# Performance work log

Hardware: AMD Instinct MI355X
Metric: run time of the kernel (lower is better)

## Reference

```python
import jax, jax.numpy as jnp
import numpy as np

N_HEAD, D_K, D_V = 8, 64, 64
TEMP = 20.0
EPS = 1e-12  # F.normalize default eps


def setup_inputs() -> dict:
    key = jax.random.key(0)
    ks = jax.random.split(key, 5)
    bs_q, bs_k, len_q, len_k, d_model = 32, 32, 100, 100, 512
    return {
        "q": jax.random.normal(ks[0], (bs_q, len_q, d_model), jnp.float32),
        "k": jax.random.normal(ks[1], (bs_k, len_k, d_model), jnp.float32),
        "v": jax.random.normal(ks[2], (bs_k, len_k, N_HEAD * D_V), jnp.float32),
        "w_qs": jax.random.normal(ks[3], (N_HEAD * D_K, d_model), jnp.float32) * 0.02,
        "w_ks": jax.random.normal(ks[4], (N_HEAD * D_K, d_model), jnp.float32) * 0.02,
    }


def _l2norm(x):
    return x / jnp.maximum(jnp.linalg.norm(x, axis=-1, keepdims=True), EPS)


def reference(q, k, v, w_qs, w_ks):
    bs_q, len_q, _ = q.shape
    bs_k, len_k, _ = k.shape
    # Linear projections (no bias), then the module's raw view (reshape, no transpose)
    qh = (q @ w_qs.T).reshape(bs_q, N_HEAD, len_q, D_K)
    kh = (k @ w_ks.T).reshape(bs_k, N_HEAD, len_k, D_K)
    vh = v.reshape(bs_k, N_HEAD, len_k, D_V)
    # cosine-similarity scores: L2-normalize q and k along d_k
    qn = _l2norm(qh)
    kn = _l2norm(kh)
    # every q batch element vs every k batch element: [bs_q, bs_k, h, len_q, len_k]
    attn = jnp.einsum("qhld,khmd->qkhlm", qn, kn)
    attn = jax.nn.relu(attn) * TEMP
    attn = jax.nn.softmax(attn, axis=-1)
    out = jnp.einsum("qkhlm,khmd->qkhld", attn, vh)
    # per-i: [bs_k, h, len_q, d_v] -> transpose(1,2) -> reshape, stacked at dim=1
    out = out.transpose(1, 0, 3, 2, 4).reshape(bs_k, bs_q, len_q, N_HEAD * D_V)
    return out
```

## Files before the change

kernel.cpp:

```cpp
#include <hip/hip_runtime.h>
#include <math.h>

typedef short bf16x8 __attribute__((ext_vector_type(8)));
typedef float f32x4  __attribute__((ext_vector_type(4)));
typedef float f32x16 __attribute__((ext_vector_type(16)));
typedef unsigned u32x4 __attribute__((ext_vector_type(4)));

#define TEMP 20.0f

__device__ __forceinline__ ushort f2bf(float f) {
    unsigned u = __float_as_uint(f);
    u = (u + 0x7FFFu + ((u >> 16) & 1u)) >> 16;
    return (ushort)u;
}

__device__ __forceinline__ bf16x8 cvt8(const float4* p) {
    float4 a = p[0], b = p[1];
    bf16x8 r;
    r[0] = (short)f2bf(a.x); r[1] = (short)f2bf(a.y);
    r[2] = (short)f2bf(a.z); r[3] = (short)f2bf(a.w);
    r[4] = (short)f2bf(b.x); r[5] = (short)f2bf(b.y);
    r[6] = (short)f2bf(b.z); r[7] = (short)f2bf(b.w);
    return r;
}

__global__ __launch_bounds__(256) void prep(const float* __restrict__ wq,
                                            const float* __restrict__ wk,
                                            const float* __restrict__ v,
                                            ushort* __restrict__ Wq,
                                            ushort* __restrict__ Wk,
                                            ushort* __restrict__ Vt) {
    __shared__ float T[100 * 65];
    const int b = blockIdx.x, t = threadIdx.x;
    if (b < 256) {
        const float* src = (b < 128) ? wq : wk;
        ushort* dst = (b < 128) ? Wq : Wk;
        const int idx = (b & 127) * 2048 + t * 8;
        *(bf16x8*)(dst + idx) = cvt8((const float4*)(src + idx));
        return;
    }
    const int bb = b - 256;
    const float* in = v + (size_t)(bb >> 3) * 51200 + (bb & 7) * 6400;
    for (int i = t; i < 6400; i += 256) T[(i >> 6) * 65 + (i & 63)] = in[i];
    __syncthreads();
    const int n = t >> 2, kc = (t & 3) * 32;
    unsigned* outw = (unsigned*)(Vt + (((size_t)bb * 64 + n) * 128 + kc));
#pragma unroll
    for (int i = 0; i < 16; ++i) {
        int c0 = kc + 2 * i, c1 = c0 + 1;
        int p0 = (c0 & ~12) | ((c0 & 4) << 1) | ((c0 & 8) >> 1);
        int p1 = (c1 & ~12) | ((c1 & 4) << 1) | ((c1 & 8) >> 1);
        unsigned lo = (p0 < 100) ? (unsigned)f2bf(T[p0 * 65 + n]) : 0u;
        unsigned hi = (p1 < 100) ? (unsigned)f2bf(T[p1 * 65 + n]) : 0u;
        outw[i] = lo | (hi << 16);
    }
}

__global__ __launch_bounds__(256) void proj_norm(const float* __restrict__ Aq,
                                                 const float* __restrict__ Ak,
                                                 const ushort* __restrict__ Wqb,
                                                 const ushort* __restrict__ Wkb,
                                                 ushort* __restrict__ Oq,
                                                 ushort* __restrict__ Ok) {
    const float* A = blockIdx.z ? Ak : Aq;
    const ushort* W = blockIdx.z ? Wkb : Wqb;
    ushort* Out = blockIdx.z ? Ok : Oq;

    const int lane = threadIdx.x & 63, w = threadIdx.x >> 6;
    const int l15 = lane & 15, quad = lane >> 4;
    const int mtile = blockIdx.x;
    const int chunk = blockIdx.y * 4 + w;
    const int m = mtile * 16 + l15;

    f32x4 acc[4];
#pragma unroll
    for (int nt = 0; nt < 4; ++nt) acc[nt] = (f32x4)(0.f);

    const float* arow = A + (size_t)m * 512 + quad * 8;
    const ushort* wbase = W + (size_t)(chunk * 64 + l15) * 512 + quad * 8;
#pragma unroll 2
    for (int k0 = 0; k0 < 512; k0 += 32) {
        bf16x8 af = cvt8((const float4*)(arow + k0));
#pragma unroll
        for (int nt = 0; nt < 4; ++nt) {
            bf16x8 bf = *(const bf16x8*)(wbase + nt * (16 * 512) + k0);
            acc[nt] = __builtin_amdgcn_mfma_f32_16x16x32_bf16(af, bf, acc[nt], 0, 0, 0);
        }
    }
#pragma unroll
    for (int reg = 0; reg < 4; ++reg) {
        float ss = 0.f;
#pragma unroll
        for (int nt = 0; nt < 4; ++nt) ss += acc[nt][reg] * acc[nt][reg];
#pragma unroll
        for (int o = 8; o >= 1; o >>= 1) ss += __shfl_xor(ss, o);
        float inv = 1.0f / fmaxf(sqrtf(ss), 1e-12f);
        int row = mtile * 16 + quad * 4 + reg;
#pragma unroll
        for (int nt = 0; nt < 4; ++nt)
            Out[(size_t)row * 512 + chunk * 64 + nt * 16 + l15] =
                f2bf(acc[nt][reg] * inv);
    }
}

__global__ __launch_bounds__(256) void attn32(const ushort* __restrict__ Pqn,
                                              const ushort* __restrict__ Pkn,
                                              const ushort* __restrict__ Vt,
                                              float* __restrict__ out) {
    const int bid = blockIdx.x;
    const int blk = (bid & 7) * 1024 + (bid >> 3);
    const int bk = blk >> 8, bq = (blk >> 3) & 31, h = blk & 7;

    const int lane = threadIdx.x & 63;
    const int w = threadIdx.x >> 6;
    const int l31 = lane & 31, hi = lane >> 5;

    const ushort* Qb = Pqn + (size_t)bq * 51200 + h * 6400;
    const ushort* Kb = Pkn + (size_t)bk * 51200 + h * 6400;
    const ushort* Vb = Vt + (size_t)(bk * 8 + h) * 8192;

    bf16x8 qf[4];
    const ushort* qrow = Qb + (w * 32 + l31) * 64 + hi * 8;
#pragma unroll
    for (int kc = 0; kc < 4; ++kc) qf[kc] = *(const bf16x8*)(qrow + kc * 16);

    f32x16 sacc[4];
#pragma unroll
    for (int kt = 0; kt < 4; ++kt) sacc[kt] = (f32x16)(0.f);

    const ushort* krow = Kb + l31 * 64 + hi * 8;
#pragma unroll
    for (int kc = 0; kc < 4; ++kc) {
        bf16x8 kf[4];
#pragma unroll
        for (int kt = 0; kt < 4; ++kt)
            kf[kt] = *(const bf16x8*)(krow + kt * 2048 + kc * 16);
#pragma unroll
        for (int kt = 0; kt < 4; ++kt)
            sacc[kt] = __builtin_amdgcn_mfma_f32_32x32x16_bf16(kf[kt], qf[kc], sacc[kt], 0, 0, 0);
    }

    const ushort* vrow = Vb + l31 * 128 + hi * 8;
    bf16x8 vf0 = *(const bf16x8*)(vrow);
    bf16x8 vf1 = *(const bf16x8*)(vrow + 4096);

    float mx0 = 0.f, mx1 = 0.f;
#pragma unroll
    for (int kt = 0; kt < 3; ++kt)
#pragma unroll
        for (int r = 0; r < 16; ++r) {
            float t = fmaxf(sacc[kt][r], 0.f);
            sacc[kt][r] = t;
            if (r & 1) mx1 = fmaxf(mx1, t); else mx0 = fmaxf(mx0, t);
        }
    if (hi == 0) {
#pragma unroll
        for (int r = 0; r < 4; ++r) {
            float t = fmaxf(sacc[3][r], 0.f);
            sacc[3][r] = t;
            if (r & 1) mx1 = fmaxf(mx1, t); else mx0 = fmaxf(mx0, t);
        }
    }
#pragma unroll
    for (int r = 4; r < 16; ++r) sacc[3][r] = 0.f;
    float mx = fmaxf(mx0, mx1);
    mx = fmaxf(mx, __shfl_xor(mx, 32));
    const float mT = mx * TEMP;
    float s0 = 0.f, s1 = 0.f, s2 = 0.f, s3 = 0.f;
#pragma unroll
    for (int kt = 0; kt < 3; ++kt)
#pragma unroll
        for (int r = 0; r < 16; ++r) {
            float e = __expf(fmaf(sacc[kt][r], TEMP, -mT));
            sacc[kt][r] = e;
            if ((r & 3) == 0) s0 += e; else if ((r & 3) == 1) s1 += e;
            else if ((r & 3) == 2) s2 += e; else s3 += e;
        }
    if (hi == 0) {
#pragma unroll
        for (int r = 0; r < 4; ++r) {
            float e = __expf(fmaf(sacc[3][r], TEMP, -mT));
            sacc[3][r] = e;
            s0 += e;
        }
    } else {
#pragma unroll
        for (int r = 0; r < 4; ++r) sacc[3][r] = 0.f;
    }
    float sum = (s0 + s1) + (s2 + s3);
    sum += __shfl_xor(sum, 32);
    const float inv = 1.0f / sum;

    f32x16 oacc0 = (f32x16)(0.f), oacc1 = (f32x16)(0.f);
#pragma unroll
    for (int ks = 0; ks < 7; ++ks) {
        const int kt = ks >> 1, tt = (ks & 1) * 8;
        unsigned d0, d1, d2, d3;
        asm("v_cvt_pk_bf16_f32 %0, %1, %2" : "=v"(d0) : "v"(sacc[kt][tt + 0]), "v"(sacc[kt][tt + 1]));
        asm("v_cvt_pk_bf16_f32 %0, %1, %2" : "=v"(d1) : "v"(sacc[kt][tt + 2]), "v"(sacc[kt][tt + 3]));
        asm("v_cvt_pk_bf16_f32 %0, %1, %2" : "=v"(d2) : "v"(sacc[kt][tt + 4]), "v"(sacc[kt][tt + 5]));
        asm("v_cvt_pk_bf16_f32 %0, %1, %2" : "=v"(d3) : "v"(sacc[kt][tt + 6]), "v"(sacc[kt][tt + 7]));
        u32x4 pw; pw[0] = d0; pw[1] = d1; pw[2] = d2; pw[3] = d3;
        bf16x8 pf = __builtin_bit_cast(bf16x8, pw);

        bf16x8 nv0, nv1;
        if (ks < 6) {
            nv0 = *(const bf16x8*)(vrow + (ks + 1) * 16);
            nv1 = *(const bf16x8*)(vrow + 4096 + (ks + 1) * 16);
        }
        oacc0 = __builtin_amdgcn_mfma_f32_32x32x16_bf16(vf0, pf, oacc0, 0, 0, 0);
        oacc1 = __builtin_amdgcn_mfma_f32_32x32x16_bf16(vf1, pf, oacc1, 0, 0, 0);
        if (ks < 6) { vf0 = nv0; vf1 = nv1; }
    }

    const int q = w * 32 + l31;
    if (q < 100) {
        float* po = out + ((size_t)(bk * 32 + bq) * 100 + q) * 512 + h * 64 + hi * 4;
#pragma unroll
        for (int g = 0; g < 4; ++g) {
            float4 v0 = {oacc0[4 * g + 0] * inv, oacc0[4 * g + 1] * inv,
                         oacc0[4 * g + 2] * inv, oacc0[4 * g + 3] * inv};
            *(float4*)(po + 8 * g) = v0;
            float4 v1 = {oacc1[4 * g + 0] * inv, oacc1[4 * g + 1] * inv,
                         oacc1[4 * g + 2] * inv, oacc1[4 * g + 3] * inv};
            *(float4*)(po + 32 + 8 * g) = v1;
        }
    }
}

extern "C" void kernel_launch(void* const* d_in, const int* in_sizes, int n_in,
                              void* d_out, int out_size, void* d_ws, size_t ws_size,
                              hipStream_t stream) {
    const float* q  = (const float*)d_in[0];
    const float* k  = (const float*)d_in[1];
    const float* v  = (const float*)d_in[2];
    const float* wq = (const float*)d_in[3];
    const float* wk = (const float*)d_in[4];
    float* out = (float*)d_out;

    ushort* Pqn = (ushort*)d_ws;
    ushort* Pkn = Pqn + 1703936;
    ushort* Vt  = Pkn + 1703936;

    ushort* Wqb = (ushort*)d_out + ((size_t)out_size / 2) - 524288;
    ushort* Wkb = Wqb + 262144;

    prep<<<512, 256, 0, stream>>>(wq, wk, v, Wqb, Wkb, Vt);
    proj_norm<<<dim3(200, 2, 2), 256, 0, stream>>>(q, k, Wqb, Wkb, Pqn, Pkn);
    attn32<<<8192, 256, 0, stream>>>(Pqn, Pkn, Vt, out);
}
```

Measured before the change: 380.4 us.

## Stage attention output through swizzled LDS for coalesced row writes; precast q/k

The attention kernel now runs one 512-thread block per (k-batch, q-batch) pair, with the 8 heads mapped to 8 waves. It loops over four 32-row query tiles and stages each tile's output in XOR-swizzled shared memory, so the output rows go to global memory as contiguous coalesced chunks instead of scattered 256-byte head segments. Separately, the prep kernel now converts q and k to bf16 ahead of time, so the projection kernel loads bf16 directly instead of converting fp32 inside its K loop. The cost is 64KB of LDS per block, fewer and larger blocks, a serial tile loop with block-wide barriers, and an extra pass that writes and rereads q/k through scratch space in the tail of the output buffer.

```diff
diff --git a/kernel.cpp b/kernel.cpp
--- a/kernel.cpp
+++ b/kernel.cpp
@@ -26,9 +26,13 @@
 
 __global__ __launch_bounds__(256) void prep(const float* __restrict__ wq,
                                             const float* __restrict__ wk,
+                                            const float* __restrict__ q,
+                                            const float* __restrict__ k,
                                             const float* __restrict__ v,
                                             ushort* __restrict__ Wq,
                                             ushort* __restrict__ Wk,
+                                            ushort* __restrict__ Aq,
+                                            ushort* __restrict__ Ak,
                                             ushort* __restrict__ Vt) {
     __shared__ float T[100 * 65];
     const int b = blockIdx.x, t = threadIdx.x;
@@ -39,7 +43,14 @@
         *(bf16x8*)(dst + idx) = cvt8((const float4*)(src + idx));
         return;
     }
-    const int bb = b - 256;
+    if (b < 1856) {
+        const float* src = (b < 1056) ? q : k;
+        ushort* dst = (b < 1056) ? Aq : Ak;
+        const int idx = ((b < 1056 ? b - 256 : b - 1056)) * 2048 + t * 8;
+        *(bf16x8*)(dst + idx) = cvt8((const float4*)(src + idx));
+        return;
+    }
+    const int bb = b - 1856;
     const float* in = v + (size_t)(bb >> 3) * 51200 + (bb & 7) * 6400;
     for (int i = t; i < 6400; i += 256) T[(i >> 6) * 65 + (i & 63)] = in[i];
     __syncthreads();
@@ -56,13 +67,13 @@
     }
 }
 
-__global__ __launch_bounds__(256) void proj_norm(const float* __restrict__ Aq,
-                                                 const float* __restrict__ Ak,
+__global__ __launch_bounds__(256) void proj_norm(const ushort* __restrict__ Abq,
+                                                 const ushort* __restrict__ Abk,
                                                  const ushort* __restrict__ Wqb,
                                                  const ushort* __restrict__ Wkb,
                                                  ushort* __restrict__ Oq,
                                                  ushort* __restrict__ Ok) {
-    const float* A = blockIdx.z ? Ak : Aq;
+    const ushort* A = blockIdx.z ? Abk : Abq;
     const ushort* W = blockIdx.z ? Wkb : Wqb;
     ushort* Out = blockIdx.z ? Ok : Oq;
 
@@ -76,11 +87,11 @@
 #pragma unroll
     for (int nt = 0; nt < 4; ++nt) acc[nt] = (f32x4)(0.f);
 
-    const float* arow = A + (size_t)m * 512 + quad * 8;
+    const ushort* arow = A + (size_t)m * 512 + quad * 8;
     const ushort* wbase = W + (size_t)(chunk * 64 + l15) * 512 + quad * 8;
 #pragma unroll 2
     for (int k0 = 0; k0 < 512; k0 += 32) {
-        bf16x8 af = cvt8((const float4*)(arow + k0));
+        bf16x8 af = *(const bf16x8*)(arow + k0);
 #pragma unroll
         for (int nt = 0; nt < 4; ++nt) {
             bf16x8 bf = *(const bf16x8*)(wbase + nt * (16 * 512) + k0);
@@ -103,128 +114,151 @@
     }
 }
 
-__global__ __launch_bounds__(256) void attn32(const ushort* __restrict__ Pqn,
+__global__ __launch_bounds__(512) void attn8h(const ushort* __restrict__ Pqn,
                                               const ushort* __restrict__ Pkn,
                                               const ushort* __restrict__ Vt,
                                               float* __restrict__ out) {
+    __shared__ float T[16384];
+
     const int bid = blockIdx.x;
-    const int blk = (bid & 7) * 1024 + (bid >> 3);
-    const int bk = blk >> 8, bq = (blk >> 3) & 31, h = blk & 7;
-
-    const int lane = threadIdx.x & 63;
-    const int w = threadIdx.x >> 6;
+    const int blk = (bid & 7) * 128 + (bid >> 3);
+    const int bk = blk >> 5, bq = blk & 31;
+
+    const int t = threadIdx.x;
+    const int lane = t & 63;
+    const int h = t >> 6;
     const int l31 = lane & 31, hi = lane >> 5;
 
     const ushort* Qb = Pqn + (size_t)bq * 51200 + h * 6400;
     const ushort* Kb = Pkn + (size_t)bk * 51200 + h * 6400;
     const ushort* Vb = Vt + (size_t)(bk * 8 + h) * 8192;
-
-    bf16x8 qf[4];
-    const ushort* qrow = Qb + (w * 32 + l31) * 64 + hi * 8;
-#pragma unroll
-    for (int kc = 0; kc < 4; ++kc) qf[kc] = *(const bf16x8*)(qrow + kc * 16);
-
-    f32x16 sacc[4];
-#pragma unroll
-    for (int kt = 0; kt < 4; ++kt) sacc[kt] = (f32x16)(0.f);
-
     const ushort* krow = Kb + l31 * 64 + hi * 8;
-#pragma unroll
-    for (int kc = 0; kc < 4; ++kc) {
-        bf16x8 kf[4];
-#pragma unroll
-        for (int kt = 0; kt < 4; ++kt)
-            kf[kt] = *(const bf16x8*)(krow + kt * 2048 + kc * 16);
-#pragma unroll
-        for (int kt = 0; kt < 4; ++kt)
-            sacc[kt] = __builtin_amdgcn_mfma_f32_32x32x16_bf16(kf[kt], qf[kc], sacc[kt], 0, 0, 0);
-    }
-
     const ushort* vrow = Vb + l31 * 128 + hi * 8;
-    bf16x8 vf0 = *(const bf16x8*)(vrow);
-    bf16x8 vf1 = *(const bf16x8*)(vrow + 4096);
-
-    float mx0 = 0.f, mx1 = 0.f;
-#pragma unroll
-    for (int kt = 0; kt < 3; ++kt)
-#pragma unroll
-        for (int r = 0; r < 16; ++r) {
-            float t = fmaxf(sacc[kt][r], 0.f);
-            sacc[kt][r] = t;
-            if (r & 1) mx1 = fmaxf(mx1, t); else mx0 = fmaxf(mx0, t);
-        }
-    if (hi == 0) {
-#pragma unroll
-        for (int r = 0; r < 4; ++r) {
-            float t = fmaxf(sacc[3][r], 0.f);
-            sacc[3][r] = t;
-            if (r & 1) mx1 = fmaxf(mx1, t); else mx0 = fmaxf(mx0, t);
-        }
-    }
-#pragma unroll
-    for (int r = 4; r < 16; ++r) sacc[3][r] = 0.f;
-    float mx = fmaxf(mx0, mx1);
-    mx = fmaxf(mx, __shfl_xor(mx, 32));
-    const float mT = mx * TEMP;
-    float s0 = 0.f, s1 = 0.f, s2 = 0.f, s3 = 0.f;
-#pragma unroll
-    for (int kt = 0; kt < 3; ++kt)
-#pragma unroll
-        for (int r = 0; r < 16; ++r) {
-            float e = __expf(fmaf(sacc[kt][r], TEMP, -mT));
-            sacc[kt][r] = e;
-            if ((r & 3) == 0) s0 += e; else if ((r & 3) == 1) s1 += e;
-            else if ((r & 3) == 2) s2 += e; else s3 += e;
-        }
-    if (hi == 0) {
-#pragma unroll
-        for (int r = 0; r < 4; ++r) {
-            float e = __expf(fmaf(sacc[3][r], TEMP, -mT));
-            sacc[3][r] = e;
-            s0 += e;
-        }
-    } else {
-#pragma unroll
-        for (int r = 0; r < 4; ++r) sacc[3][r] = 0.f;
-    }
-    float sum = (s0 + s1) + (s2 + s3);
-    sum += __shfl_xor(sum, 32);
-    const float inv = 1.0f / sum;
-
-    f32x16 oacc0 = (f32x16)(0.f), oacc1 = (f32x16)(0.f);
-#pragma unroll
-    for (int ks = 0; ks < 7; ++ks) {
-        const int kt = ks >> 1, tt = (ks & 1) * 8;
-        unsigned d0, d1, d2, d3;
-        asm("v_cvt_pk_bf16_f32 %0, %1, %2" : "=v"(d0) : "v"(sacc[kt][tt + 0]), "v"(sacc[kt][tt + 1]));
-        asm("v_cvt_pk_bf16_f32 %0, %1, %2" : "=v"(d1) : "v"(sacc[kt][tt + 2]), "v"(sacc[kt][tt + 3]));
-        asm("v_cvt_pk_bf16_f32 %0, %1, %2" : "=v"(d2) : "v"(sacc[kt][tt + 4]), "v"(sacc[kt][tt + 5]));
-        asm("v_cvt_pk_bf16_f32 %0, %1, %2" : "=v"(d3) : "v"(sacc[kt][tt + 6]), "v"(sacc[kt][tt + 7]));
-        u32x4 pw; pw[0] = d0; pw[1] = d1; pw[2] = d2; pw[3] = d3;
-        bf16x8 pf = __builtin_bit_cast(bf16x8, pw);
-
-        bf16x8 nv0, nv1;
-        if (ks < 6) {
-            nv0 = *(const bf16x8*)(vrow + (ks + 1) * 16);
-            nv1 = *(const bf16x8*)(vrow + 4096 + (ks + 1) * 16);
-        }
-        oacc0 = __builtin_amdgcn_mfma_f32_32x32x16_bf16(vf0, pf, oacc0, 0, 0, 0);
-        oacc1 = __builtin_amdgcn_mfma_f32_32x32x16_bf16(vf1, pf, oacc1, 0, 0, 0);
-        if (ks < 6) { vf0 = nv0; vf1 = nv1; }
-    }
-
-    const int q = w * 32 + l31;
-    if (q < 100) {
-        float* po = out + ((size_t)(bk * 32 + bq) * 100 + q) * 512 + h * 64 + hi * 4;
-#pragma unroll
-        for (int g = 0; g < 4; ++g) {
-            float4 v0 = {oacc0[4 * g + 0] * inv, oacc0[4 * g + 1] * inv,
-                         oacc0[4 * g + 2] * inv, oacc0[4 * g + 3] * inv};
-            *(float4*)(po + 8 * g) = v0;
-            float4 v1 = {oacc1[4 * g + 0] * inv, oacc1[4 * g + 1] * inv,
-                         oacc1[4 * g + 2] * inv, oacc1[4 * g + 3] * inv};
-            *(float4*)(po + 32 + 8 * g) = v1;
-        }
+    float* const outB = out + (size_t)(bk * 32 + bq) * 51200;
+
+#pragma unroll 1
+    for (int qt = 0; qt < 4; ++qt) {
+        const int qr = qt * 32 + l31;
+        const ushort* qrow = Qb + (qr < 100 ? qr : 99) * 64 + hi * 8;
+        bf16x8 qf[4];
+#pragma unroll
+        for (int kc = 0; kc < 4; ++kc) qf[kc] = *(const bf16x8*)(qrow + kc * 16);
+
+        f32x16 sacc[4];
+#pragma unroll
+        for (int kt = 0; kt < 4; ++kt) sacc[kt] = (f32x16)(0.f);
+
+#pragma unroll
+        for (int kc = 0; kc < 4; ++kc) {
+            bf16x8 kf[4];
+#pragma unroll
+            for (int kt = 0; kt < 4; ++kt)
+                kf[kt] = *(const bf16x8*)(krow + kt * 2048 + kc * 16);
+#pragma unroll
+            for (int kt = 0; kt < 4; ++kt)
+                sacc[kt] = __builtin_amdgcn_mfma_f32_32x32x16_bf16(kf[kt], qf[kc], sacc[kt], 0, 0, 0);
+        }
+
+        bf16x8 vf0 = *(const bf16x8*)(vrow);
+        bf16x8 vf1 = *(const bf16x8*)(vrow + 4096);
+
+        float mx0 = 0.f, mx1 = 0.f;
+#pragma unroll
+        for (int kt = 0; kt < 3; ++kt)
+#pragma unroll
+            for (int r = 0; r < 16; ++r) {
+                float tv = fmaxf(sacc[kt][r], 0.f);
+                sacc[kt][r] = tv;
+                if (r & 1) mx1 = fmaxf(mx1, tv); else mx0 = fmaxf(mx0, tv);
+            }
+        if (hi == 0) {
+#pragma unroll
+            for (int r = 0; r < 4; ++r) {
+                float tv = fmaxf(sacc[3][r], 0.f);
+                sacc[3][r] = tv;
+                if (r & 1) mx1 = fmaxf(mx1, tv); else mx0 = fmaxf(mx0, tv);
+            }
+        }
+#pragma unroll
+        for (int r = 4; r < 16; ++r) sacc[3][r] = 0.f;
+        float mx = fmaxf(mx0, mx1);
+        mx = fmaxf(mx, __shfl_xor(mx, 32));
+        const float mT = mx * TEMP;
+        float s0 = 0.f, s1 = 0.f, s2 = 0.f, s3 = 0.f;
+#pragma unroll
+        for (int kt = 0; kt < 3; ++kt)
+#pragma unroll
+            for (int r = 0; r < 16; ++r) {
+                float e = __expf(fmaf(sacc[kt][r], TEMP, -mT));
+                sacc[kt][r] = e;
+                if ((r & 3) == 0) s0 += e; else if ((r & 3) == 1) s1 += e;
+                else if ((r & 3) == 2) s2 += e; else s3 += e;
+            }
+        if (hi == 0) {
+#pragma unroll
+            for (int r = 0; r < 4; ++r) {
+                float e = __expf(fmaf(sacc[3][r], TEMP, -mT));
+                sacc[3][r] = e;
+                s0 += e;
+            }
+        } else {
+#pragma unroll
+            for (int r = 0; r < 4; ++r) sacc[3][r] = 0.f;
+        }
+        float sum = (s0 + s1) + (s2 + s3);
+        sum += __shfl_xor(sum, 32);
+        const float inv = 1.0f / sum;
+
+        f32x16 oacc0 = (f32x16)(0.f), oacc1 = (f32x16)(0.f);
+#pragma unroll
+        for (int ks = 0; ks < 7; ++ks) {
+            const int kt = ks >> 1, tt = (ks & 1) * 8;
+            unsigned d0, d1, d2, d3;
+            asm("v_cvt_pk_bf16_f32 %0, %1, %2" : "=v"(d0) : "v"(sacc[kt][tt + 0]), "v"(sacc[kt][tt + 1]));
+            asm("v_cvt_pk_bf16_f32 %0, %1, %2" : "=v"(d1) : "v"(sacc[kt][tt + 2]), "v"(sacc[kt][tt + 3]));
+            asm("v_cvt_pk_bf16_f32 %0, %1, %2" : "=v"(d2) : "v"(sacc[kt][tt + 4]), "v"(sacc[kt][tt + 5]));
+            asm("v_cvt_pk_bf16_f32 %0, %1, %2" : "=v"(d3) : "v"(sacc[kt][tt + 6]), "v"(sacc[kt][tt + 7]));
+            u32x4 pw; pw[0] = d0; pw[1] = d1; pw[2] = d2; pw[3] = d3;
+            bf16x8 pf = __builtin_bit_cast(bf16x8, pw);
+
+            bf16x8 nv0, nv1;
+            if (ks < 6) {
+                nv0 = *(const bf16x8*)(vrow + (ks + 1) * 16);
+                nv1 = *(const bf16x8*)(vrow + 4096 + (ks + 1) * 16);
+            }
+            oacc0 = __builtin_amdgcn_mfma_f32_32x32x16_bf16(vf0, pf, oacc0, 0, 0, 0);
+            oacc1 = __builtin_amdgcn_mfma_f32_32x32x16_bf16(vf1, pf, oacc1, 0, 0, 0);
+            if (ks < 6) { vf0 = nv0; vf1 = nv1; }
+        }
+
+        {
+            const int swz = (l31 & 7) << 4;
+            char* rowp = (char*)T + l31 * 2048;
+#pragma unroll
+            for (int g = 0; g < 4; ++g) {
+                int cb0 = h * 256 + g * 32 + hi * 16;
+                float4 v0 = {oacc0[4 * g + 0] * inv, oacc0[4 * g + 1] * inv,
+                             oacc0[4 * g + 2] * inv, oacc0[4 * g + 3] * inv};
+                *(float4*)(rowp + (cb0 ^ swz)) = v0;
+                int cb1 = cb0 + 128;
+                float4 v1 = {oacc1[4 * g + 0] * inv, oacc1[4 * g + 1] * inv,
+                             oacc1[4 * g + 2] * inv, oacc1[4 * g + 3] * inv};
+                *(float4*)(rowp + (cb1 ^ swz)) = v1;
+            }
+        }
+        __syncthreads();
+
+        {
+            float* gb = outB + qt * 16384;
+            const int nIter = (qt < 3) ? 8 : 1;
+            for (int i = 0; i < nIter; ++i) {
+                int off = i * 8192 + t * 16;
+                int qrl = off >> 11, cb = off & 2047;
+                float4 val = *(float4*)((char*)T + qrl * 2048 + (cb ^ ((qrl & 7) << 4)));
+                *(float4*)((char*)gb + off) = val;
+            }
+        }
+        if (qt < 3) __syncthreads();
     }
 }
 
@@ -242,10 +276,13 @@
     ushort* Pkn = Pqn + 1703936;
     ushort* Vt  = Pkn + 1703936;
 
-    ushort* Wqb = (ushort*)d_out + ((size_t)out_size / 2) - 524288;
+    ushort* tail = (ushort*)d_out + ((size_t)out_size / 2) - 3801088;
+    ushort* Wqb = tail;
     ushort* Wkb = Wqb + 262144;
-
-    prep<<<512, 256, 0, stream>>>(wq, wk, v, Wqb, Wkb, Vt);
-    proj_norm<<<dim3(200, 2, 2), 256, 0, stream>>>(q, k, Wqb, Wkb, Pqn, Pkn);
-    attn32<<<8192, 256, 0, stream>>>(Pqn, Pkn, Vt, out);
-}
+    ushort* Abq = Wkb + 262144;
+    ushort* Abk = Abq + 1638400;
+
+    prep<<<2112, 256, 0, stream>>>(wq, wk, q, k, v, Wqb, Wkb, Abq, Abk, Vt);
+    proj_norm<<<dim3(200, 2, 2), 256, 0, stream>>>(Abq, Abk, Wqb, Wkb, Pqn, Pkn);
+    attn8h<<<1024, 512, 0, stream>>>(Pqn, Pkn, Vt, out);
+}
```

Measured after the change: 338.3 us. 1.12x faster.
